# Performance work log

Measured on AMD Instinct MI355X. Metric: run time of the kernel, lower is better.

Reference implementation:

```python
import jax, jax.numpy as jnp
import numpy as np

C1, C2, C3, C4, C5 = 20, 100, 500, 2000, 10000
FEAT, B = 512, 8192
# parent maps (stand-ins for l1_to_l2..l4_to_l5 group lists): child c -> parent c // fanout
P5 = jnp.arange(C5) // 5   # l5 class -> l4 group
P4 = jnp.arange(C4) // 4   # l4 class -> l3 group
P3 = jnp.arange(C3) // 5   # l3 class -> l2 group
P2 = jnp.arange(C2) // 5   # l2 class -> l1 group


def _l2norm(w):
    # F.normalize(w, p=2, dim=1)
    return w / jnp.maximum(jnp.linalg.norm(w, axis=1, keepdims=True), 1e-12)


def _jsd(p, q, eps=1e-8):
    # Jensen-Shannon divergence between row-wise distributions, mean over batch
    m = 0.5 * (p + q)
    log_m = jnp.log(m + eps)
    kl_pm = jnp.sum(p * (jnp.log(p + eps) - log_m), axis=1)
    kl_qm = jnp.sum(q * (jnp.log(q + eps) - log_m), axis=1)
    return jnp.mean(0.5 * (kl_pm + kl_qm))


def setup_inputs() -> dict:
    key = jax.random.key(0)
    k = jax.random.split(key, 8)
    s = 0.02
    return {
        "x": jax.random.normal(k[0], (B, FEAT), jnp.float32),
        "targets": jax.random.randint(k[1], (B,), 0, C5, jnp.int32),
        "W1": jax.random.normal(k[2], (C1, FEAT), jnp.float32) * s,
        "b1": jnp.zeros((C1,), jnp.float32),
        "W2": jax.random.normal(k[3], (C2, FEAT), jnp.float32) * s,
        "b2": jnp.zeros((C2,), jnp.float32),
        "W3": jax.random.normal(k[4], (C3, FEAT), jnp.float32) * s,
        "b3": jnp.zeros((C3,), jnp.float32),
        "W4": jax.random.normal(k[5], (C4, FEAT), jnp.float32) * s,
        "b4": jnp.zeros((C4,), jnp.float32),
        "W5": jax.random.normal(k[6], (C5, FEAT), jnp.float32) * s,
        "b5": jnp.zeros((C5,), jnp.float32),
    }


def reference(x, targets, W1, b1, W2, b2, W3, b3, W4, b4, W5, b5):
    # row-normalized classifier weights (second F.normalize in the original is idempotent)
    w1, w2, w3, w4, w5 = (_l2norm(W1), _l2norm(W2), _l2norm(W3), _l2norm(W4), _l2norm(W5))
    l1 = x @ w1.T + b1
    l2 = x @ w2.T + b2
    l3 = x @ w3.T + b3
    l4 = x @ w4.T + b4
    l5 = x @ w5.T + b5  # [B, C5]

    # cross-entropy on finest level logits
    logp5 = jax.nn.log_softmax(l5, axis=1)
    ce_loss = -jnp.mean(jnp.take_along_axis(logp5, targets[:, None].astype(jnp.int32), axis=1)[:, 0])

    p1 = jax.nn.softmax(l1, axis=1)
    p2 = jax.nn.softmax(l2, axis=1)
    p3 = jax.nn.softmax(l3, axis=1)
    p4 = jax.nn.softmax(l4, axis=1)
    p5 = jax.nn.softmax(l5, axis=1)

    # hierarchy-aggregated weights: segment-sum child rows, renormalize, cosine vs parent
    def agg_cos(parent_w, child_w, seg, num_seg):
        hat = _l2norm(jax.ops.segment_sum(child_w, seg, num_segments=num_seg))
        return jnp.mean(jnp.sum(parent_w * hat, axis=1))  # rows are unit norm -> cosine

    l2_w_45 = agg_cos(w4, w5, P5, C4)
    l2_w_34 = agg_cos(w3, w4, P4, C3)
    l2_w_23 = agg_cos(w2, w3, P3, C2)
    l2_w_12 = agg_cos(w1, w2, P2, C1)

    # hierarchy-aggregated probabilities: column segment-sums, then JSD vs parent
    def agg_prob(child_p, seg, num_seg):
        return jax.ops.segment_sum(child_p.T, seg, num_segments=num_seg).T

    jsd_45 = _jsd(agg_prob(p5, P5, C4), p4)
    jsd_34 = _jsd(agg_prob(p4, P4, C3), p3)
    jsd_23 = _jsd(agg_prob(p3, P3, C2), p2)
    jsd_12 = _jsd(agg_prob(p2, P2, C1), p1)

    loss = ce_loss + (jsd_45 + jsd_34 + jsd_23 + jsd_12) - (l2_w_45 + l2_w_34 + l2_w_23 + l2_w_12)
    return p5, loss
```

## Files before the change

kernel.cpp:

```cpp
#include <hip/hip_runtime.h>
#include <hip/hip_bf16.h>
#include <stdint.h>

typedef unsigned short u16;
typedef __bf16 bf16x8 __attribute__((ext_vector_type(8)));
typedef float f32x4 __attribute__((ext_vector_type(4)));
typedef unsigned int u32x4 __attribute__((ext_vector_type(4)));

#define FEAT 512
#define BATCH 8192
#define NC1 20
#define NC2 100
#define NC3 500
#define NC4 2000
#define NC5 10000
#define NCAT 2620
#define LDP 2624
#define NTOT 12620
#define WN_BLOCKS 3155
#define CAST_BLOCKS 2048

__device__ inline u16 f2bf(float f) {
    unsigned int u = __builtin_bit_cast(unsigned int, f);
    unsigned int r = (u + 0x7FFFu + ((u >> 16) & 1u)) >> 16;
    return (u16)r;
}
__device__ inline float bfu(u16 u) {
    return __builtin_bit_cast(float, (unsigned int)u << 16);
}

__device__ inline float waveReduceSum(float v) {
    #pragma unroll
    for (int off = 32; off > 0; off >>= 1) v += __shfl_xor(v, off);
    return v;
}
__device__ inline float waveReduceMax(float v) {
    #pragma unroll
    for (int off = 32; off > 0; off >>= 1) v = fmaxf(v, __shfl_xor(v, off));
    return v;
}
__device__ inline float blockReduceSum(float v, float* sh) {
    int t = threadIdx.x;
    v = waveReduceSum(v);
    __syncthreads();
    if ((t & 63) == 0) sh[t >> 6] = v;
    __syncthreads();
    return sh[0] + sh[1] + sh[2] + sh[3];
}
__device__ inline float blockReduceMax(float v, float* sh) {
    int t = threadIdx.x;
    v = waveReduceMax(v);
    __syncthreads();
    if ((t & 63) == 0) sh[t >> 6] = v;
    __syncthreads();
    return fmaxf(fmaxf(sh[0], sh[1]), fmaxf(sh[2], sh[3]));
}

__device__ inline void gload16(const void* g, void* l) {
    __builtin_amdgcn_global_load_lds((const __attribute__((address_space(1))) void*)g,
                                     (__attribute__((address_space(3))) void*)l, 16, 0, 0);
}


__global__ __launch_bounds__(256) void prep(const float* __restrict__ x, u16* __restrict__ xb,
                                            const float* __restrict__ W1, const float* __restrict__ b1,
                                            const float* __restrict__ W2, const float* __restrict__ b2,
                                            const float* __restrict__ W3, const float* __restrict__ b3,
                                            const float* __restrict__ W4, const float* __restrict__ b4,
                                            const float* __restrict__ W5, const float* __restrict__ b5,
                                            u16* __restrict__ wb, float* __restrict__ biascat) {
    int bid = blockIdx.x;
    if (bid < WN_BLOCKS) {
        int r = bid * 4 + (threadIdx.x >> 6);
        if (r >= NTOT) return;
        int t = threadIdx.x & 63;
        const float* W; const float* b; int lr;
        if      (r < 20)   { W = W1; b = b1; lr = r; }
        else if (r < 120)  { W = W2; b = b2; lr = r - 20; }
        else if (r < 620)  { W = W3; b = b3; lr = r - 120; }
        else if (r < 2620) { W = W4; b = b4; lr = r - 620; }
        else               { W = W5; b = b5; lr = r - 2620; }
        const float* p = W + (size_t)lr * FEAT + t * 8;
        float v[8]; float ss = 0.f;
        #pragma unroll
        for (int j = 0; j < 8; ++j) { v[j] = p[j]; ss += v[j] * v[j]; }
        ss = waveReduceSum(ss);
        float inv = 1.0f / fmaxf(sqrtf(ss), 1e-12f);
        union { u16 u[8]; uint4 q; } o;
        #pragma unroll
        for (int j = 0; j < 8; ++j) o.u[j] = f2bf(v[j] * inv);
        ((uint4*)(wb + (size_t)r * FEAT))[t] = o.q;
        if (t == 0) biascat[r] = b[lr];
    } else {
        int i = (bid - WN_BLOCKS) * 256 + threadIdx.x;
        const float* p = x + (size_t)i * 8;
        union { u16 u[8]; uint4 v; } o;
        #pragma unroll
        for (int j = 0; j < 8; ++j) o.u[j] = f2bf(p[j]);
        ((uint4*)xb)[i] = o.v;
    }
}


#define BM 256
#define BN 256
#define BK 64
#define KITERS (FEAT / BK)

__global__ __launch_bounds__(512, 2) void gemm_all(const u16* __restrict__ A, const u16* __restrict__ Bw,
                                                   const float* __restrict__ bias,
                                                   u16* __restrict__ pcat, u16* __restrict__ l5b,
                                                   float* __restrict__ pmax, float* __restrict__ psum) {
    __shared__ u16 sAB[2][2 * BM * BK];
    const int t = threadIdx.x;
    const int lane = t & 63, wid = t >> 6;
    const int lane15 = lane & 15, q = lane >> 4;
    const int wr = wid >> 2, wcol = wid & 3;

    int nwg = gridDim.x * gridDim.y;
    int lid = blockIdx.y * gridDim.x + blockIdx.x;
    int cpx = nwg >> 3;
    int swz = (lid & 7) * cpx + (lid >> 3);
    int bx = swz % gridDim.x, by = swz / gridDim.x;
    const int r0 = bx * BM, c0 = by * BN;

    f32x4 acc[8][4];
    #pragma unroll
    for (int m = 0; m < 8; ++m)
        #pragma unroll
        for (int n = 0; n < 4; ++n) acc[m][n] = f32x4{0.f, 0.f, 0.f, 0.f};

    auto stage = [&](int kt, int buf) {
        char* base = (char*)sAB[buf];
        #pragma unroll
        for (int p = 0; p < 8; ++p) {
            int chunk = p * 512 + t;
            int row = chunk >> 3, blk = chunk & 7;
            int srck = 8 * (blk ^ (row & 7));
            const u16* g;
            if (p < 4) {
                g = A + (size_t)(r0 + row) * FEAT + kt + srck;
            } else {
                int brow = c0 + (row - 256); if (brow >= NTOT) brow = NTOT - 1;
                g = Bw + (size_t)brow * FEAT + kt + srck;
            }
            gload16(g, base + (size_t)chunk * 16);
        }
    };

    stage(0, 0);
    stage(BK, 1);
    for (int ki = 0; ki < KITERS; ++ki) {
        if (ki + 1 < KITERS) { asm volatile("s_waitcnt vmcnt(8)" ::: "memory"); }
        else                 { asm volatile("s_waitcnt vmcnt(0)" ::: "memory"); }
        __builtin_amdgcn_sched_barrier(0);
        __builtin_amdgcn_s_barrier();
        __builtin_amdgcn_sched_barrier(0);
        char* sAb = (char*)sAB[ki & 1];
        char* sBb = sAb + BM * BK * 2;
        #pragma unroll
        for (int ks = 0; ks < 2; ++ks) {
            const int kko = ks * 4 + q;
            bf16x8 af[8], bv[4];
            #pragma unroll
            for (int m = 0; m < 8; ++m) {
                int row = wr * 128 + m * 16 + lane15;
                af[m] = *reinterpret_cast<const bf16x8*>(sAb + row * 128 + 16 * (kko ^ (row & 7)));
            }
            #pragma unroll
            for (int n = 0; n < 4; ++n) {
                int row = wcol * 64 + n * 16 + lane15;
                bv[n] = *reinterpret_cast<const bf16x8*>(sBb + row * 128 + 16 * (kko ^ (row & 7)));
            }
            __builtin_amdgcn_s_setprio(1);
            #pragma unroll
            for (int m = 0; m < 8; ++m)
                #pragma unroll
                for (int n = 0; n < 4; ++n)
                    acc[m][n] = __builtin_amdgcn_mfma_f32_16x16x32_bf16(bv[n], af[m], acc[m][n], 0, 0, 0);
            __builtin_amdgcn_s_setprio(0);
        }
        __builtin_amdgcn_sched_barrier(0);
        __builtin_amdgcn_s_barrier();
        __builtin_amdgcn_sched_barrier(0);
        if (ki + 2 < KITERS) stage((ki + 2) * BK, ki & 1);
    }

    bool vld[4], svld[4]; int cb[4];
    #pragma unroll
    for (int n = 0; n < 4; ++n) {
        cb[n] = c0 + wcol * 64 + n * 16 + q * 4;
        vld[n] = (cb[n] < NTOT);
        svld[n] = vld[n] && (cb[n] >= NCAT);
        if (vld[n]) {
            float b0 = bias[cb[n]], b1 = bias[cb[n] + 1], b2 = bias[cb[n] + 2], b3 = bias[cb[n] + 3];
            #pragma unroll
            for (int m = 0; m < 8; ++m) {
                acc[m][n][0] += b0; acc[m][n][1] += b1;
                acc[m][n][2] += b2; acc[m][n][3] += b3;
            }
        }
    }

    if (by >= 10) {
        float* fmx = (float*)sAB;
        float* fsm = fmx + 1024;
        float bm[8];
        #pragma unroll
        for (int m = 0; m < 8; ++m) {
            float v = -1e30f;
            #pragma unroll
            for (int n = 0; n < 4; ++n)
                if (svld[n]) {
                    #pragma unroll
                    for (int j = 0; j < 4; ++j) v = fmaxf(v, acc[m][n][j]);
                }
            v = fmaxf(v, __shfl_xor(v, 16));
            v = fmaxf(v, __shfl_xor(v, 32));
            bm[m] = v;
        }
        if (lane < 16) {
            #pragma unroll
            for (int m = 0; m < 8; ++m)
                fmx[(wr * 128 + m * 16 + lane15) * 4 + wcol] = bm[m];
        }
        __syncthreads();
        #pragma unroll
        for (int m = 0; m < 8; ++m) {
            int row = wr * 128 + m * 16 + lane15;
            bm[m] = fmaxf(fmaxf(fmx[row * 4], fmx[row * 4 + 1]),
                          fmaxf(fmx[row * 4 + 2], fmx[row * 4 + 3]));
        }
        float sm[8];
        #pragma unroll
        for (int m = 0; m < 8; ++m) {
            float s = 0.f;
            #pragma unroll
            for (int n = 0; n < 4; ++n)
                if (svld[n]) {
                    #pragma unroll
                    for (int j = 0; j < 4; ++j) s += __expf(acc[m][n][j] - bm[m]);
                }
            s += __shfl_xor(s, 16);
            s += __shfl_xor(s, 32);
            sm[m] = s;
        }
        if (lane < 16) {
            #pragma unroll
            for (int m = 0; m < 8; ++m)
                fsm[(wr * 128 + m * 16 + lane15) * 4 + wcol] = sm[m];
        }
        __syncthreads();
        if (t < 256) {
            float m4 = fmaxf(fmaxf(fmx[t * 4], fmx[t * 4 + 1]), fmaxf(fmx[t * 4 + 2], fmx[t * 4 + 3]));
            float s4 = fsm[t * 4] + fsm[t * 4 + 1] + fsm[t * 4 + 2] + fsm[t * 4 + 3];
            size_t idx = (size_t)(r0 + t) * 40 + (by - 10);
            pmax[idx] = m4;
            psum[idx] = s4;
        }
    }

    #pragma unroll
    for (int m = 0; m < 8; ++m) {
        int row = r0 + wr * 128 + m * 16 + lane15;
        #pragma unroll
        for (int n = 0; n < 4; ++n) {
            if (vld[n]) {
                union { u16 u[4]; uint2 v; } pk;
                #pragma unroll
                for (int j = 0; j < 4; ++j) pk.u[j] = f2bf(acc[m][n][j]);
                u16* dst = (cb[n] < NCAT)
                    ? &pcat[(size_t)row * LDP + cb[n]]
                    : &l5b[(size_t)row * NC5 + (cb[n] - NCAT)];
                *reinterpret_cast<uint2*>(dst) = pk.v;
            }
        }
    }
}


__global__ __launch_bounds__(256) void probs_all(const u16* __restrict__ l5b, float* __restrict__ out,
                                                 const u16* __restrict__ pcat,
                                                 const float* __restrict__ pmax, const float* __restrict__ psum,
                                                 int nct, const int* __restrict__ tgt,
                                                 float* __restrict__ cerow,
                                                 float* __restrict__ j12, float* __restrict__ j23,
                                                 float* __restrict__ j34, float* __restrict__ j45) {
    __shared__ u16 P5[NC5];
    __shared__ float PC[LDP];
    __shared__ float sh[4];
    __shared__ float shls;
    int b = blockIdx.x, t = threadIdx.x;
    float* orow = out + (size_t)b * NC5;
    const u16* lrow = l5b + (size_t)b * NC5;
    const u16* prow = pcat + (size_t)b * LDP;

    if (t < 64) {
        float pm = (t < nct) ? pmax[(size_t)b * nct + t] : -1e30f;
        float ps = (t < nct) ? psum[(size_t)b * nct + t] : 0.f;
        float gm = waveReduceMax(pm);
        float s = waveReduceSum(ps * __expf(pm - gm));
        if (t == 0) {
            float ls = gm + __logf(s);
            shls = ls;
            int tg = tgt[b];
            cerow[b] = -(bfu(lrow[tg]) - ls);
        }
    }
    for (int c = t; c < LDP / 8; c += 256) {
        u32x4 raw = __builtin_nontemporal_load(&((const u32x4*)prow)[c]);
        const u16* rp = (const u16*)&raw;
        #pragma unroll
        for (int k = 0; k < 8; ++k) PC[c * 8 + k] = bfu(rp[k]);
    }
    __syncthreads();
    float ls = shls;

    for (int c = t; c < NC5 / 8; c += 256) {
        u32x4 raw = __builtin_nontemporal_load(&((const u32x4*)lrow)[c]);
        const u16* rp = (const u16*)&raw;
        f32x4 p0, p1;
        #pragma unroll
        for (int k = 0; k < 4; ++k) p0[k] = __expf(bfu(rp[k]) - ls);
        #pragma unroll
        for (int k = 0; k < 4; ++k) p1[k] = __expf(bfu(rp[4 + k]) - ls);
        __builtin_nontemporal_store(p0, &((f32x4*)orow)[c * 2]);
        __builtin_nontemporal_store(p1, &((f32x4*)orow)[c * 2 + 1]);
        union { u16 u[8]; uint4 v; } pk;
        #pragma unroll
        for (int k = 0; k < 4; ++k) pk.u[k] = f2bf(p0[k]);
        #pragma unroll
        for (int k = 0; k < 4; ++k) pk.u[4 + k] = f2bf(p1[k]);
        ((uint4*)P5)[c] = pk.v;
    }
    __syncthreads();

    auto softmax_seg = [&](int off, int C) {
        float m = -1e30f;
        for (int c = t; c < C; c += 256) m = fmaxf(m, PC[off + c]);
        m = blockReduceMax(m, sh);
        float s = 0.f;
        for (int c = t; c < C; c += 256) { float e = __expf(PC[off + c] - m); PC[off + c] = e; s += e; }
        s = blockReduceSum(s, sh);
        float inv = 1.0f / s;
        for (int c = t; c < C; c += 256) PC[off + c] *= inv;
    };
    softmax_seg(0, NC1);
    softmax_seg(20, NC2);
    softmax_seg(120, NC3);
    softmax_seg(620, NC4);
    __syncthreads();

    {
        float klpm = 0.f, klqm = 0.f;
        for (int g = t; g < NC4; g += 256) {
            float qv = 0.f;
            #pragma unroll
            for (int f = 0; f < 5; ++f) qv += bfu(P5[5 * g + f]);
            float pp = PC[620 + g];
            float mm = 0.5f * (qv + pp);
            float lm = __logf(mm + 1e-8f);
            klpm += qv * (__logf(qv + 1e-8f) - lm);
            klqm += pp * (__logf(pp + 1e-8f) - lm);
        }
        float tot = blockReduceSum(0.5f * (klpm + klqm), sh);
        if (t == 0) j45[b] = tot;
    }
    auto jsd_seg = [&](int childOff, int fan, int parentOff, int nPar, float* dst) {
        float klpm = 0.f, klqm = 0.f;
        for (int g = t; g < nPar; g += 256) {
            float qv = 0.f;
            for (int f = 0; f < fan; ++f) qv += PC[childOff + g * fan + f];
            float pp = PC[parentOff + g];
            float mm = 0.5f * (qv + pp);
            float lm = __logf(mm + 1e-8f);
            klpm += qv * (__logf(qv + 1e-8f) - lm);
            klqm += pp * (__logf(pp + 1e-8f) - lm);
        }
        float tot = blockReduceSum(0.5f * (klpm + klqm), sh);
        if (t == 0) dst[b] = tot;
    };
    jsd_seg(620, 4, 120, NC3, j34);
    jsd_seg(120, 5, 20, NC2, j23);
    jsd_seg(20, 5, 0, NC1, j12);
}


__global__ __launch_bounds__(64) void wcos_all(const u16* __restrict__ wb,
                                               float* __restrict__ c45, float* __restrict__ c34,
                                               float* __restrict__ c23, float* __restrict__ c12) {
    int g = blockIdx.x; int t = threadIdx.x;
    int pOff, cOff, fan, j; float* dst;
    if      (g < 2000) { pOff = 620; cOff = 2620; fan = 5; dst = c45; j = g; }
    else if (g < 2500) { pOff = 120; cOff = 620;  fan = 4; dst = c34; j = g - 2000; }
    else if (g < 2600) { pOff = 20;  cOff = 120;  fan = 5; dst = c23; j = g - 2500; }
    else               { pOff = 0;   cOff = 20;   fan = 5; dst = c12; j = g - 2600; }

    float hat[8] = {0, 0, 0, 0, 0, 0, 0, 0};
    for (int c = 0; c < fan; ++c) {
        const uint4 raw = ((const uint4*)(wb + (size_t)(cOff + j * fan + c) * FEAT))[t];
        const u16* rp = (const u16*)&raw;
        #pragma unroll
        for (int i = 0; i < 8; ++i) hat[i] += bfu(rp[i]);
    }
    float hs = 0.f;
    #pragma unroll
    for (int i = 0; i < 8; ++i) hs += hat[i] * hat[i];
    hs = waveReduceSum(hs);
    float hinv = 1.0f / fmaxf(sqrtf(hs), 1e-12f);
    const uint4 praw = ((const uint4*)(wb + (size_t)(pOff + j) * FEAT))[t];
    const u16* pp = (const u16*)&praw;
    float dot = 0.f;
    #pragma unroll
    for (int i = 0; i < 8; ++i) dot += bfu(pp[i]) * hat[i];
    dot = waveReduceSum(dot);
    if (t == 0) dst[j] = dot * hinv;
}

__global__ __launch_bounds__(256) void finalize(const float* __restrict__ ce, const float* __restrict__ j45,
                                                const float* __restrict__ j34, const float* __restrict__ j23,
                                                const float* __restrict__ j12, const float* __restrict__ c45,
                                                const float* __restrict__ c34, const float* __restrict__ c23,
                                                const float* __restrict__ c12, float* __restrict__ lossOut) {
    __shared__ float sh[4];
    auto meanArr = [&](const float* a, int n) {
        float s = 0.f;
        for (int i = threadIdx.x; i < n; i += 256) s += a[i];
        s = blockReduceSum(s, sh);
        return s / n;
    };
    float loss = meanArr(ce, BATCH);
    loss += meanArr(j45, BATCH) + meanArr(j34, BATCH) + meanArr(j23, BATCH) + meanArr(j12, BATCH);
    loss -= meanArr(c45, NC4) + meanArr(c34, NC3) + meanArr(c23, NC2) + meanArr(c12, NC1);
    if (threadIdx.x == 0) *lossOut = loss;
}


extern "C" void kernel_launch(void* const* d_in, const int* in_sizes, int n_in,
                              void* d_out, int out_size, void* d_ws, size_t ws_size,
                              hipStream_t stream) {
    const float* x  = (const float*)d_in[0];
    const int*   tg = (const int*)d_in[1];
    const float* W1 = (const float*)d_in[2];  const float* b1 = (const float*)d_in[3];
    const float* W2 = (const float*)d_in[4];  const float* b2 = (const float*)d_in[5];
    const float* W3 = (const float*)d_in[6];  const float* b3 = (const float*)d_in[7];
    const float* W4 = (const float*)d_in[8];  const float* b4 = (const float*)d_in[9];
    const float* W5 = (const float*)d_in[10]; const float* b5 = (const float*)d_in[11];
    float* out = (float*)d_out;

    const int NCT = 40;

    char* ws = (char*)d_ws;
    size_t off = 0;
    auto alloc = [&](size_t bytes) { void* p = ws + off; off = (off + bytes + 255) & ~(size_t)255; return p; };
    u16*   xb      = (u16*)alloc((size_t)BATCH * FEAT * 2);
    u16*   wb      = (u16*)alloc((size_t)NTOT * FEAT * 2);
    float* biascat = (float*)alloc((size_t)NTOT * 4);
    u16*   pcat    = (u16*)alloc((size_t)BATCH * LDP * 2);
    u16*   l5b     = (u16*)alloc((size_t)BATCH * NC5 * 2);
    float* pmax    = (float*)alloc((size_t)BATCH * NCT * 4);
    float* psum    = (float*)alloc((size_t)BATCH * NCT * 4);
    float* cerow   = (float*)alloc((size_t)BATCH * 4);
    float* j45     = (float*)alloc((size_t)BATCH * 4);
    float* j34     = (float*)alloc((size_t)BATCH * 4);
    float* j23     = (float*)alloc((size_t)BATCH * 4);
    float* j12     = (float*)alloc((size_t)BATCH * 4);
    float* c45     = (float*)alloc((size_t)NC4 * 4);
    float* c34     = (float*)alloc((size_t)NC3 * 4);
    float* c23     = (float*)alloc((size_t)NC2 * 4);
    float* c12     = (float*)alloc((size_t)NC1 * 4);

    prep<<<WN_BLOCKS + CAST_BLOCKS, 256, 0, stream>>>(x, xb, W1, b1, W2, b2, W3, b3, W4, b4, W5, b5,
                                                      wb, biascat);

    gemm_all<<<dim3(BATCH / BM, (NTOT + BN - 1) / BN), 512, 0, stream>>>(
        xb, wb, biascat, pcat, l5b, pmax, psum);

    probs_all<<<BATCH, 256, 0, stream>>>(l5b, out, pcat, pmax, psum, NCT, tg, cerow,
                                         j12, j23, j34, j45);

    wcos_all<<<NC4 + NC3 + NC2 + NC1, 64, 0, stream>>>(wb, c45, c34, c23, c12);

    finalize<<<1, 256, 0, stream>>>(cerow, j45, j34, j23, j12, c45, c34, c23, c12,
                                    out + (size_t)BATCH * NC5);
}
```

Baseline: 391.9 us.

## Shrink GEMM tile to 128x256x32 with k-major LDS layout and higher occupancy

The fused logits GEMM moves from 256x256 tiles with BK=64 to 128x256 tiles with BK=32. It halves the accumulator count per wave and raises the launch-bounds occupancy hint from 2 to 4 blocks per CU. The shared-memory layout changes from a row-major XOR-swizzled layout to a k-block-major layout, with the wait counts adjusted to match. The aim is more concurrency and better latency hiding, at the cost of less operand reuse per tile, twice as many k-iterations with barriers, and possible LDS bank conflicts in the new layout. The host grid dimensions must also change to match the smaller BM, and that change is not visible here.

After: 457.6 us. 1.17x slower.

```diff
diff --git a/kernel.cpp b/kernel.cpp
--- a/kernel.cpp
+++ b/kernel.cpp
@@ -102,20 +102,21 @@
 }
 
 
-#define BM 256
+#define BM 128
 #define BN 256
-#define BK 64
+#define BK 32
 #define KITERS (FEAT / BK)
-
-__global__ __launch_bounds__(512, 2) void gemm_all(const u16* __restrict__ A, const u16* __restrict__ Bw,
+#define CHUNKS ((BM + BN) * BK / 8)
+
+__global__ __launch_bounds__(512, 4) void gemm_all(const u16* __restrict__ A, const u16* __restrict__ Bw,
                                                    const float* __restrict__ bias,
                                                    u16* __restrict__ pcat, u16* __restrict__ l5b,
                                                    float* __restrict__ pmax, float* __restrict__ psum) {
-    __shared__ u16 sAB[2][2 * BM * BK];
+    __shared__ u16 sAB[2][(BM + BN) * BK];
     const int t = threadIdx.x;
     const int lane = t & 63, wid = t >> 6;
     const int lane15 = lane & 15, q = lane >> 4;
-    const int wr = wid >> 2, wcol = wid & 3;
+    const int wrow = wid >> 2, wcol = wid & 3;
 
     int nwg = gridDim.x * gridDim.y;
     int lid = blockIdx.y * gridDim.x + blockIdx.x;
@@ -124,62 +125,58 @@
     int bx = swz % gridDim.x, by = swz / gridDim.x;
     const int r0 = bx * BM, c0 = by * BN;
 
-    f32x4 acc[8][4];
-    #pragma unroll
-    for (int m = 0; m < 8; ++m)
+    f32x4 acc[4][4];
+    #pragma unroll
+    for (int m = 0; m < 4; ++m)
         #pragma unroll
         for (int n = 0; n < 4; ++n) acc[m][n] = f32x4{0.f, 0.f, 0.f, 0.f};
 
     auto stage = [&](int kt, int buf) {
         char* base = (char*)sAB[buf];
         #pragma unroll
-        for (int p = 0; p < 8; ++p) {
-            int chunk = p * 512 + t;
-            int row = chunk >> 3, blk = chunk & 7;
-            int srck = 8 * (blk ^ (row & 7));
+        for (int p = 0; p < 3; ++p) {
+            int c = p * 512 + t;
             const u16* g;
-            if (p < 4) {
-                g = A + (size_t)(r0 + row) * FEAT + kt + srck;
+            if (p == 0) {
+                int row = c & 127, blk = c >> 7;
+                g = A + (size_t)(r0 + row) * FEAT + kt + blk * 8;
             } else {
-                int brow = c0 + (row - 256); if (brow >= NTOT) brow = NTOT - 1;
-                g = Bw + (size_t)brow * FEAT + kt + srck;
+                int cc = c - 512;
+                int row = cc & 255, blk = cc >> 8;
+                int brow = c0 + row; if (brow >= NTOT) brow = NTOT - 1;
+                g = Bw + (size_t)brow * FEAT + kt + blk * 8;
             }
-            gload16(g, base + (size_t)chunk * 16);
+            gload16(g, base + (size_t)c * 16);
         }
     };
 
     stage(0, 0);
     stage(BK, 1);
     for (int ki = 0; ki < KITERS; ++ki) {
-        if (ki + 1 < KITERS) { asm volatile("s_waitcnt vmcnt(8)" ::: "memory"); }
+        if (ki + 1 < KITERS) { asm volatile("s_waitcnt vmcnt(3)" ::: "memory"); }
         else                 { asm volatile("s_waitcnt vmcnt(0)" ::: "memory"); }
         __builtin_amdgcn_sched_barrier(0);
         __builtin_amdgcn_s_barrier();
         __builtin_amdgcn_sched_barrier(0);
-        char* sAb = (char*)sAB[ki & 1];
-        char* sBb = sAb + BM * BK * 2;
-        #pragma unroll
-        for (int ks = 0; ks < 2; ++ks) {
-            const int kko = ks * 4 + q;
-            bf16x8 af[8], bv[4];
-            #pragma unroll
-            for (int m = 0; m < 8; ++m) {
-                int row = wr * 128 + m * 16 + lane15;
-                af[m] = *reinterpret_cast<const bf16x8*>(sAb + row * 128 + 16 * (kko ^ (row & 7)));
-            }
-            #pragma unroll
-            for (int n = 0; n < 4; ++n) {
-                int row = wcol * 64 + n * 16 + lane15;
-                bv[n] = *reinterpret_cast<const bf16x8*>(sBb + row * 128 + 16 * (kko ^ (row & 7)));
-            }
-            __builtin_amdgcn_s_setprio(1);
-            #pragma unroll
-            for (int m = 0; m < 8; ++m)
-                #pragma unroll
-                for (int n = 0; n < 4; ++n)
-                    acc[m][n] = __builtin_amdgcn_mfma_f32_16x16x32_bf16(bv[n], af[m], acc[m][n], 0, 0, 0);
-            __builtin_amdgcn_s_setprio(0);
-        }
+        char* base = (char*)sAB[ki & 1];
+        bf16x8 af[4], bv[4];
+        #pragma unroll
+        for (int m = 0; m < 4; ++m) {
+            int row = wrow * 64 + m * 16 + lane15;
+            af[m] = *reinterpret_cast<const bf16x8*>(base + q * 2048 + row * 16);
+        }
+        #pragma unroll
+        for (int n = 0; n < 4; ++n) {
+            int row = wcol * 64 + n * 16 + lane15;
+            bv[n] = *reinterpret_cast<const bf16x8*>(base + 8192 + q * 4096 + row * 16);
+        }
+        __builtin_amdgcn_s_setprio(1);
+        #pragma unroll
+        for (int m = 0; m < 4; ++m)
+            #pragma unroll
+            for (int n = 0; n < 4; ++n)
+                acc[m][n] = __builtin_amdgcn_mfma_f32_16x16x32_bf16(bv[n], af[m], acc[m][n], 0, 0, 0);
+        __builtin_amdgcn_s_setprio(0);
         __builtin_amdgcn_sched_barrier(0);
         __builtin_amdgcn_s_barrier();
         __builtin_amdgcn_sched_barrier(0);
@@ -195,7 +192,7 @@
         if (vld[n]) {
             float b0 = bias[cb[n]], b1 = bias[cb[n] + 1], b2 = bias[cb[n] + 2], b3 = bias[cb[n] + 3];
             #pragma unroll
-            for (int m = 0; m < 8; ++m) {
+            for (int m = 0; m < 4; ++m) {
                 acc[m][n][0] += b0; acc[m][n][1] += b1;
                 acc[m][n][2] += b2; acc[m][n][3] += b3;
             }
@@ -204,10 +201,10 @@
 
     if (by >= 10) {
         float* fmx = (float*)sAB;
-        float* fsm = fmx + 1024;
-        float bm[8];
-        #pragma unroll
-        for (int m = 0; m < 8; ++m) {
+        float* fsm = fmx + 512;
+        float bm[4];
+        #pragma unroll
+        for (int m = 0; m < 4; ++m) {
             float v = -1e30f;
             #pragma unroll
             for (int n = 0; n < 4; ++n)
@@ -221,19 +218,19 @@
         }
         if (lane < 16) {
             #pragma unroll
-            for (int m = 0; m < 8; ++m)
-                fmx[(wr * 128 + m * 16 + lane15) * 4 + wcol] = bm[m];
+            for (int m = 0; m < 4; ++m)
+                fmx[(wrow * 64 + m * 16 + lane15) * 4 + wcol] = bm[m];
         }
         __syncthreads();
         #pragma unroll
-        for (int m = 0; m < 8; ++m) {
-            int row = wr * 128 + m * 16 + lane15;
+        for (int m = 0; m < 4; ++m) {
+            int row = wrow * 64 + m * 16 + lane15;
             bm[m] = fmaxf(fmaxf(fmx[row * 4], fmx[row * 4 + 1]),
                           fmaxf(fmx[row * 4 + 2], fmx[row * 4 + 3]));
         }
-        float sm[8];
-        #pragma unroll
-        for (int m = 0; m < 8; ++m) {
+        float sm[4];
+        #pragma unroll
+        for (int m = 0; m < 4; ++m) {
             float s = 0.f;
             #pragma unroll
             for (int n = 0; n < 4; ++n)
@@ -247,11 +244,11 @@
         }
         if (lane < 16) {
             #pragma unroll
-            for (int m = 0; m < 8; ++m)
-                fsm[(wr * 128 + m * 16 + lane15) * 4 + wcol] = sm[m];
+            for (int m = 0; m < 4; ++m)
+                fsm[(wrow * 64 + m * 16 + lane15) * 4 + wcol] = sm[m];
         }
         __syncthreads();
-        if (t < 256) {
+        if (t < 128) {
             float m4 = fmaxf(fmaxf(fmx[t * 4], fmx[t * 4 + 1]), fmaxf(fmx[t * 4 + 2], fmx[t * 4 + 3]));
             float s4 = fsm[t * 4] + fsm[t * 4 + 1] + fsm[t * 4 + 2] + fsm[t * 4 + 3];
             size_t idx = (size_t)(r0 + t) * 40 + (by - 10);
@@ -261,8 +258,8 @@
     }
 
     #pragma unroll
-    for (int m = 0; m < 8; ++m) {
-        int row = r0 + wr * 128 + m * 16 + lane15;
+    for (int m = 0; m < 4; ++m) {
+        int row = r0 + wrow * 64 + m * 16 + lane15;
         #pragma unroll
         for (int n = 0; n < 4; ++n) {
             if (vld[n]) {
```
